# Kernel tuning notes

Measured on AMD Instinct MI355X. Metric: run time of the kernel, lower is better.

## Reference

```python
import jax, jax.numpy as jnp
import numpy as np

N_NODES = 100000
N_EDGES = 1000000
NODE_DIM = 64
EDGE_DIM = 32
N_LAYERS = 4
NUM_GAUSS = EDGE_DIM // 2
HIDDEN = 2 * NODE_DIM
NUM_GRAPHS = 64
VOCAB = 100


def setup_inputs() -> dict:
    key = jax.random.key(0)
    ks = jax.random.split(key, 16)
    atoms = jax.random.randint(ks[0], (N_NODES,), 0, VOCAB, dtype=jnp.int32)
    edge_index = jax.random.randint(ks[1], (2, N_EDGES), 0, N_NODES, dtype=jnp.int32)
    coordinates = jax.random.normal(ks[2], (N_NODES, 3), dtype=jnp.float32) * 2.0
    is_receptor = jax.random.randint(ks[3], (N_NODES,), 0, 2, dtype=jnp.int32)
    batch_ids = jnp.sort(jax.random.randint(ks[4], (N_NODES,), 0, NUM_GRAPHS, dtype=jnp.int32))
    cat_dim = 2 * NODE_DIM + EDGE_DIM  # 160
    node_embed_w = jax.random.normal(ks[5], (VOCAB, NODE_DIM), dtype=jnp.float32) * 0.02
    subunit_embed_w = jax.random.normal(ks[6], (2, EDGE_DIM // 2), dtype=jnp.float32) * 0.02
    W1 = jax.random.normal(ks[7], (N_LAYERS, cat_dim, HIDDEN), dtype=jnp.float32) * (cat_dim ** -0.5)
    b1 = jnp.zeros((N_LAYERS, HIDDEN), dtype=jnp.float32)
    W2 = jax.random.normal(ks[8], (N_LAYERS, HIDDEN, NODE_DIM), dtype=jnp.float32) * (HIDDEN ** -0.5)
    b2 = jnp.zeros((N_LAYERS, NODE_DIM), dtype=jnp.float32)
    fc_w = jax.random.normal(ks[9], (NODE_DIM, 1), dtype=jnp.float32) * (NODE_DIM ** -0.5)
    fc_b = jnp.zeros((1,), dtype=jnp.float32)
    return {"atoms": atoms, "edge_index": edge_index, "coordinates": coordinates,
            "is_receptor": is_receptor, "batch_ids": batch_ids,
            "node_embed_w": node_embed_w, "subunit_embed_w": subunit_embed_w,
            "W1": W1, "b1": b1, "W2": W2, "b2": b2, "fc_w": fc_w, "fc_b": fc_b}


def reference(atoms, edge_index, coordinates, is_receptor, batch_ids,
              node_embed_w, subunit_embed_w, W1, b1, W2, b2, fc_w, fc_b):
    src, dst = edge_index[0], edge_index[1]
    # node embedding
    h = node_embed_w[atoms]  # [N, D]
    # edge attributes: RBF of distance + intermolecular-kind embedding
    offset = jnp.linspace(0.0, 5.0, NUM_GAUSS, dtype=jnp.float32)
    coeff = -0.5 / float(5.0 / (NUM_GAUSS - 1)) ** 2
    dist = jnp.linalg.norm(coordinates[src] - coordinates[dst], axis=1)  # [E]
    rbf = jnp.exp(coeff * (dist[:, None] - offset[None, :]) ** 2)  # [E, G]
    kind = (is_receptor[src] != is_receptor[dst]).astype(jnp.int32)
    edge_attr = jnp.concatenate([rbf, subunit_embed_w[kind]], axis=1)  # [E, EDGE_DIM]
    # message passing layers (PyG source_to_target: h_i = h[dst], h_j = h[src], aggr at dst)
    for l in range(W1.shape[0]):
        m = jnp.concatenate([h[dst], h[src], edge_attr], axis=1)  # [E, 2D+EDGE_DIM]
        m = jax.nn.silu(m @ W1[l] + b1[l]) @ W2[l] + b2[l]  # [E, D]
        agg = jax.ops.segment_sum(m, dst, num_segments=h.shape[0])
        h = jax.nn.relu(h + agg)
    # global mean pool over graphs
    sums = jax.ops.segment_sum(h, batch_ids, num_segments=NUM_GRAPHS)
    counts = jax.ops.segment_sum(jnp.ones((h.shape[0],), h.dtype), batch_ids, num_segments=NUM_GRAPHS)
    pooled = sums / jnp.maximum(counts, 1.0)[:, None]
    out = pooled @ fc_w + fc_b  # [G, 1]
    return out.squeeze(-1)
```

## Files before the change

kernel.cpp:

```cpp
#include <hip/hip_runtime.h>
#include <hip/hip_bf16.h>
#include <math.h>

#define NODE_DIM  64
#define EDGE_DIM  32
#define NUM_GAUSS 16
#define HIDDEN    128
#define CAT_DIM   160
#define TBL_BINS  2048
#define TBL_SCALE 256.0f
#define L1ABSZ    (64 * 256)
#define L2SZ      (HIDDEN * NODE_DIM)
#define TBLSZ     (2 * TBL_BINS * 128)

#define NEG_L2E   (-1.442695040888963f)
#define NEG_LN2   (-0.6931471805599453f)

#define BKT_SH    9
#define BKT_SZ    512
#define NBKT_MAX  1024


typedef __attribute__((ext_vector_type(8))) short short8;
typedef __attribute__((ext_vector_type(4))) short short4v;
typedef __attribute__((ext_vector_type(4))) float float4v;

static __device__ __forceinline__ short f2bf(float x) {
  __hip_bfloat16 h = __float2bfloat16(x);
  return *reinterpret_cast<short*>(&h);
}
static __device__ __forceinline__ float bf2f(short s) {
  return __uint_as_float(((unsigned)(unsigned short)s) << 16);
}
static __device__ __forceinline__ float bflo(unsigned u) { return __uint_as_float(u << 16); }
static __device__ __forceinline__ float bfhi(unsigned u) { return __uint_as_float(u & 0xffff0000u); }

#if defined(__has_builtin) && __has_builtin(__builtin_amdgcn_exp2f)
static __device__ __forceinline__ float hw_exp2(float x) { return __builtin_amdgcn_exp2f(x); }
#else
static __device__ __forceinline__ float hw_exp2(float x) { return exp2f(x); }
#endif

__global__ void k_init(const int* __restrict__ atoms, const float* __restrict__ embed_w,
                       short* __restrict__ hb, int n) {
  int stride = gridDim.x * blockDim.x;
  for (int i = blockIdx.x * blockDim.x + threadIdx.x; i < n; i += stride) {
    int p = i & 63;
    int col = (p & 3) * 16 + (p >> 2);
    hb[i] = f2bf(embed_w[atoms[i >> 6] * NODE_DIM + col]);
  }
}

__global__ void k_zero_f(float* __restrict__ p, int n) {
  int stride = gridDim.x * blockDim.x;
  for (int i = blockIdx.x * blockDim.x + threadIdx.x; i < n; i += stride) p[i] = 0.f;
}
__global__ void k_zero_i(int* __restrict__ p, int n) {
  int i = blockIdx.x * blockDim.x + threadIdx.x;
  if (i < n) p[i] = 0;
}

__global__ __launch_bounds__(256) void k_edge_pre(
    const int* __restrict__ src, const int* __restrict__ dst,
    const float* __restrict__ coords, const int* __restrict__ isr,
    int* __restrict__ rec, int* __restrict__ bkt_total, int E) {
  __shared__ int h[NBKT_MAX];
  for (int i = threadIdx.x; i < NBKT_MAX; i += 256) h[i] = 0;
  __syncthreads();
  int stride = gridDim.x * blockDim.x;
  for (int e = blockIdx.x * blockDim.x + threadIdx.x; e < E; e += stride) {
    int s = src[e], d = dst[e];
    float dx = coords[s*3+0] - coords[d*3+0];
    float dy = coords[s*3+1] - coords[d*3+1];
    float dz = coords[s*3+2] - coords[d*3+2];
    float dist = sqrtf(dx*dx + dy*dy + dz*dz);
    int bin = (int)(dist * TBL_SCALE);
    bin = (bin > TBL_BINS - 1) ? TBL_BINS - 1 : bin;
    int kind = (isr[s] != isr[d]) ? 1 : 0;
    rec[e] = (s << 12) | (kind << 11) | bin;
    atomicAdd(&h[d >> BKT_SH], 1);
  }
  __syncthreads();
  for (int i = threadIdx.x; i < NBKT_MAX; i += 256)
    if (h[i]) atomicAdd(&bkt_total[i], h[i]);
}

__global__ void k_scan_buckets(const int* __restrict__ tot, int* __restrict__ base,
                               int* __restrict__ cur) {
  __shared__ int s[NBKT_MAX];
  int t = threadIdx.x;
  int v = tot[t];
  s[t] = v;
  __syncthreads();
  for (int o = 1; o < NBKT_MAX; o <<= 1) {
    int u = (t >= o) ? s[t - o] : 0;
    __syncthreads();
    s[t] += u;
    __syncthreads();
  }
  int ex = s[t] - v;
  base[t] = ex;
  cur[t]  = ex;
}

__global__ __launch_bounds__(256) void k_passA(
    const int* __restrict__ dst, const int* __restrict__ rec,
    int* __restrict__ bkt_cursor,
    int* __restrict__ tmp_rec, unsigned short* __restrict__ tmp_dl, int E) {
  __shared__ int h[NBKT_MAX];
  __shared__ int c[NBKT_MAX];
  const int tid = threadIdx.x;
  const int chunk = (E + gridDim.x - 1) / gridDim.x;
  const int c0 = blockIdx.x * chunk;
  const int c1 = (c0 + chunk < E) ? c0 + chunk : E;
  for (int i = tid; i < NBKT_MAX; i += 256) h[i] = 0;
  __syncthreads();
  for (int e = c0 + tid; e < c1; e += 256)
    atomicAdd(&h[dst[e] >> BKT_SH], 1);
  __syncthreads();
  for (int i = tid; i < NBKT_MAX; i += 256)
    c[i] = h[i] ? atomicAdd(&bkt_cursor[i], h[i]) : 0;
  __syncthreads();
  for (int e = c0 + tid; e < c1; e += 256) {
    int d = dst[e];
    int p = atomicAdd(&c[d >> BKT_SH], 1);
    tmp_rec[p] = rec[e];
    tmp_dl[p]  = (unsigned short)(d & (BKT_SZ - 1));
  }
}

__global__ __launch_bounds__(256) void k_passB(
    const int* __restrict__ tmp_rec, const unsigned short* __restrict__ tmp_dl,
    const int* __restrict__ bkt_base,
    int* __restrict__ sd_p, int* __restrict__ colptr, int* __restrict__ cnts,
    int N, int E, int nbkt) {
  __shared__ int h[BKT_SZ];
  __shared__ int cur[BKT_SZ];
  __shared__ int ps[256];
  const int tid = threadIdx.x;
  const int b = blockIdx.x;
  const int rb = bkt_base[b];
  const int re = (b == nbkt - 1) ? E : bkt_base[b + 1];

  h[tid] = 0; h[tid + 256] = 0;
  __syncthreads();
  for (int r = rb + tid; r < re; r += 256)
    atomicAdd(&h[tmp_dl[r]], 1);
  __syncthreads();

  int a0 = h[2*tid], a1 = h[2*tid + 1];
  ps[tid] = a0 + a1;
  __syncthreads();
  for (int o = 1; o < 256; o <<= 1) {
    int u = (tid >= o) ? ps[tid - o] : 0;
    __syncthreads();
    ps[tid] += u;
    __syncthreads();
  }
  int e0 = tid ? ps[tid - 1] : 0;
  int g0 = rb + e0;
  int g1 = g0 + a0;
  cur[2*tid]     = g0;
  cur[2*tid + 1] = g1;
  int node0 = b * BKT_SZ + 2*tid;
  if (node0 < N)     { colptr[node0]     = g0; cnts[node0]     = a0; }
  if (node0 + 1 < N) { colptr[node0 + 1] = g1; cnts[node0 + 1] = a1; }
  if (b == 0 && tid == 0) colptr[N] = E;
  __syncthreads();

  for (int r = rb + tid; r < re; r += 256) {
    int dl = tmp_dl[r];
    int p = atomicAdd(&cur[dl], 1);
    sd_p[p] = tmp_rec[r];
  }
}

__global__ void k_tbl(const float* __restrict__ W1, const float* __restrict__ sub_w,
                      short* __restrict__ tbl, int total) {
  int i = blockIdx.x * 256 + threadIdx.x;
  if (i >= total) return;
  int col  = i & 127;
  int idx  = i >> 7;
  int bin  = idx & (TBL_BINS - 1);
  int kind = (idx >> 11) & 1;
  int l    = idx >> 12;
  float dist = ((float)bin + 0.5f) * (1.0f / TBL_SCALE);
  const float* W1c = W1 + (size_t)l * CAT_DIM * HIDDEN + 128 * HIDDEN;
  float acc = 0.f;
  #pragma unroll
  for (int g = 0; g < 16; ++g) {
    float t = dist - (float)g * (1.0f / 3.0f);
    acc += __expf(-4.5f * t * t) * W1c[g * 128 + col];
  }
  #pragma unroll
  for (int g = 0; g < 16; ++g)
    acc += sub_w[kind * 16 + g] * W1c[(16 + g) * 128 + col];
  tbl[(size_t)idx * 128 + (col & 15) * 8 + (col >> 4)] = f2bf(acc * NEG_L2E);
}

__global__ void k_pack_w1ab(const float* __restrict__ W1, short* __restrict__ Wp, int total) {
  int i = blockIdx.x * blockDim.x + threadIdx.x;
  if (i >= total) return;
  int l = i / L1ABSZ, r = i % L1ABSZ;
  int k = r / 256, n = r % 256;
  int kp = (k & 15) * 4 + (k >> 4);
  int kt = kp >> 5, quad = (kp >> 3) & 3, j = kp & 7;
  int srow = (n < 128) ? k : 64 + k;
  int scol = (n < 128) ? n : n - 128;
  Wp[l * L1ABSZ + ((kt*4 + quad) * 256 + n) * 8 + j] =
      f2bf(W1[(size_t)l * CAT_DIM * HIDDEN + srow * HIDDEN + scol] * NEG_L2E);
}
__global__ void k_pack_w2(const float* __restrict__ W, short* __restrict__ Wp, int total) {
  int i = blockIdx.x * blockDim.x + threadIdx.x;
  if (i >= total) return;
  int l = i / L2SZ, r = i % L2SZ;
  int k = r / NODE_DIM, n = r % NODE_DIM;
  int kp = (k & 15) * 8 + (k >> 4);
  int kt = kp >> 5, quad = (kp >> 3) & 3, j = kp & 7;
  Wp[l * L2SZ + ((kt*4 + quad) * NODE_DIM + n) * 8 + j] = f2bf(W[i]);
}

__global__ __launch_bounds__(256, 4) void k_node(
    short* __restrict__ hb,
    const short* __restrict__ Sb, const int* __restrict__ cnts,
    const short* __restrict__ W2p, const float* __restrict__ b2,
    const short* __restrict__ W1abp, const float* __restrict__ b1,
    short* __restrict__ pa, short* __restrict__ pb, int N)
{
  __shared__ short ht[64 * 72];

  const int tid  = threadIdx.x;
  const int lane = tid & 63;
  const int w    = tid >> 6;
  const int quad = lane >> 4;
  const int l16  = lane & 15;
  const int base = blockIdx.x * 64 + w * 16;

  if (W2p) {
    float4v acc[4];
    #pragma unroll
    for (int nt = 0; nt < 4; ++nt) acc[nt] = (float4v)0.f;
    const int arow = base + l16;
    const bool av = arow < N;
    #pragma unroll
    for (int kt = 0; kt < 4; ++kt) {
      short8 a = av ? *(const short8*)&Sb[(size_t)arow * 128 + kt*32 + quad*8]
                    : (short8)0;
      #pragma unroll
      for (int nt = 0; nt < 4; ++nt) {
        short8 b = *(const short8*)&W2p[((kt*4 + quad) * NODE_DIM + nt*16 + l16) * 8];
        acc[nt] = __builtin_amdgcn_mfma_f32_16x16x32_bf16(a, b, acc[nt], 0, 0, 0);
      }
    }
    float bb[4];
    #pragma unroll
    for (int nt = 0; nt < 4; ++nt) bb[nt] = b2[nt*16 + l16];
    #pragma unroll
    for (int r = 0; r < 4; ++r) {
      int row  = base + quad*4 + r;
      int lrow = w*16 + quad*4 + r;
      if (row < N) {
        float cf = (float)cnts[row];
        short4v hv = *(const short4v*)&hb[(size_t)row * 64 + l16*4];
        float v0 = fmaxf(bf2f(hv[0]) + acc[0][r] + cf * bb[0], 0.f);
        float v1 = fmaxf(bf2f(hv[1]) + acc[1][r] + cf * bb[1], 0.f);
        float v2 = fmaxf(bf2f(hv[2]) + acc[2][r] + cf * bb[2], 0.f);
        float v3 = fmaxf(bf2f(hv[3]) + acc[3][r] + cf * bb[3], 0.f);
        short4v hs = {f2bf(v0), f2bf(v1), f2bf(v2), f2bf(v3)};
        *(short4v*)&hb[(size_t)row * 64 + l16*4] = hs;
        *(short4v*)&ht[lrow * 72 + l16*4] = hs;
      } else {
        *(short4v*)&ht[lrow * 72 + l16*4] = (short4v)0;
      }
    }
  } else {
    int row = base + l16;
    #pragma unroll
    for (int c = 0; c < 2; ++c) {
      int colc = quad*16 + c*8;
      short8 v = (row < N) ? *(const short8*)&hb[(size_t)row * 64 + colc] : (short8)0;
      *(short8*)&ht[(w*16 + l16) * 72 + colc] = v;
    }
  }

  if (W1abp) {
    float4v acc[16];
    #pragma unroll
    for (int nt = 0; nt < 16; ++nt) acc[nt] = (float4v)0.f;
    #pragma unroll
    for (int kt = 0; kt < 2; ++kt) {
      short8 a = *(const short8*)&ht[(w*16 + l16) * 72 + kt*32 + quad*8];
      #pragma unroll
      for (int nt = 0; nt < 16; ++nt) {
        short8 b = *(const short8*)&W1abp[((kt*4 + quad) * 256 + nt*16 + l16) * 8];
        acc[nt] = __builtin_amdgcn_mfma_f32_16x16x32_bf16(a, b, acc[nt], 0, 0, 0);
      }
    }
    float b1a[8];
    #pragma unroll
    for (int nt = 0; nt < 8; ++nt) b1a[nt] = b1[nt*16 + l16] * NEG_L2E;
    #pragma unroll
    for (int r = 0; r < 4; ++r) {
      int row = base + quad*4 + r;
      if (row < N) {
        short8 va, vb;
        #pragma unroll
        for (int nt = 0; nt < 8; ++nt) va[nt] = f2bf(acc[nt][r] + b1a[nt]);
        #pragma unroll
        for (int nt = 0; nt < 8; ++nt) vb[nt] = f2bf(acc[nt + 8][r]);
        *(short8*)&pa[(size_t)row * 128 + l16*8] = va;
        *(short8*)&pb[(size_t)row * 128 + l16*8] = vb;
      }
    }
  }
}

__global__ __launch_bounds__(256, 8) void k_gather(
    const short* __restrict__ pa, const short* __restrict__ pb,
    const short* __restrict__ tblL,
    const int* __restrict__ sd_p, const int* __restrict__ colptr,
    short* __restrict__ Sb, int N)
{
  const int W   = gridDim.x * 4;
  const int wid = blockIdx.x * 4 + (threadIdx.x >> 6);
  const int lane = threadIdx.x & 63;
  const int d2 = lane * 2;
  const int d4 = lane * 4;

  const char* pbB = (const char*)pb;
  const char* tbB = (const char*)tblL;

  for (int n = wid; n < N; n += W) {
    const int s = __builtin_amdgcn_readfirstlane(colptr[n]);
    const int e = __builtin_amdgcn_readfirstlane(colptr[n + 1]);

    unsigned up = *(const unsigned*)&pa[(size_t)n * 128 + d2];
    const float p0 = bflo(up), p1 = bfhi(up);
    float s0 = 0.f, s1 = 0.f;

    if (e > s) {
      unsigned ub0[4], ue0[4], ub1[4], ue1[4];

      auto load4 = [&](unsigned (&ub)[4], unsigned (&ue)[4], int j) {
        #pragma unroll
        for (int t = 0; t < 4; ++t) {
          int jj = (j + t < e) ? j + t : s;
          int rc = __builtin_amdgcn_readfirstlane(sd_p[jj]);
          const char* pr = pbB + ((size_t)((unsigned)rc >> 12) << 8);
          const char* tr = tbB + ((size_t)(rc & 0xfff) << 8);
          ub[t] = *(const unsigned*)(pr + d4);
          ue[t] = *(const unsigned*)(tr + d4);
        }
      };
      auto consume4 = [&](unsigned (&ub)[4], unsigned (&ue)[4], int j) {
        #pragma unroll
        for (int t = 0; t < 4; ++t) {
          if (j + t < e) {
            float y0 = p0 + bflo(ub[t]) + bflo(ue[t]);
            float y1 = p1 + bfhi(ub[t]) + bfhi(ue[t]);
            s0 += y0 * __builtin_amdgcn_rcpf(1.f + hw_exp2(y0));
            s1 += y1 * __builtin_amdgcn_rcpf(1.f + hw_exp2(y1));
          }
        }
      };

      load4(ub0, ue0, s);
      int j = s;
      for (; j + 4 < e; j += 8) {
        load4(ub1, ue1, j + 4);
        consume4(ub0, ue0, j);
        if (j + 8 < e) load4(ub0, ue0, j + 8);
        consume4(ub1, ue1, j + 4);
      }
      if (j < e) consume4(ub0, ue0, j);
    }

    s0 *= NEG_LN2;
    s1 *= NEG_LN2;
    unsigned pk = ((unsigned)(unsigned short)f2bf(s1) << 16) | (unsigned short)f2bf(s0);
    *(unsigned*)&Sb[(size_t)n * 128 + d2] = pk;
  }
}

__global__ void k_pool(const short* __restrict__ hb, const int* __restrict__ batch_ids,
                       float* __restrict__ pooled, float* __restrict__ counts, int N) {
  int lane = threadIdx.x & 63;
  int base = blockIdx.x * 64;
  float acc = 0.f;
  int   cnt = 0;
  int  gcur = -1;
  for (int n = 0; n < 64; ++n) {
    int node = base + n;
    if (node >= N) break;
    int g = batch_ids[node];
    if (g != gcur) {
      if (gcur >= 0) {
        atomicAdd(&pooled[gcur * NODE_DIM + lane], acc);
        if (lane == 0) atomicAdd(&counts[gcur], (float)cnt);
      }
      gcur = g; acc = 0.f; cnt = 0;
    }
    acc += bf2f(hb[(size_t)node * NODE_DIM + lane]);
    cnt++;
  }
  if (gcur >= 0) {
    atomicAdd(&pooled[gcur * NODE_DIM + lane], acc);
    if (lane == 0) atomicAdd(&counts[gcur], (float)cnt);
  }
}

__global__ void k_final(const float* __restrict__ pooled, const float* __restrict__ counts,
                        const float* __restrict__ fc_w, const float* __restrict__ fc_b,
                        float* __restrict__ out, int G) {
  int g = blockIdx.x * blockDim.x + threadIdx.x;
  if (g < G) {
    float acc = 0.f;
    for (int d = 0; d < NODE_DIM; ++d) {
      int col = (d & 3) * 16 + (d >> 2);
      acc += pooled[g * NODE_DIM + d] * fc_w[col];
    }
    float c = counts[g];
    if (c < 1.f) c = 1.f;
    out[g] = acc / c + fc_b[0];
  }
}

extern "C" void kernel_launch(void* const* d_in, const int* in_sizes, int n_in,
                              void* d_out, int out_size, void* d_ws, size_t ws_size,
                              hipStream_t stream) {
  const int*   atoms   = (const int*)  d_in[0];
  const int*   eidx    = (const int*)  d_in[1];
  const float* coords  = (const float*)d_in[2];
  const int*   isr     = (const int*)  d_in[3];
  const int*   batch   = (const int*)  d_in[4];
  const float* embed_w = (const float*)d_in[5];
  const float* sub_w   = (const float*)d_in[6];
  const float* W1      = (const float*)d_in[7];
  const float* b1      = (const float*)d_in[8];
  const float* W2      = (const float*)d_in[9];
  const float* b2      = (const float*)d_in[10];
  const float* fc_w    = (const float*)d_in[11];
  const float* fc_b    = (const float*)d_in[12];
  float* out = (float*)d_out;

  const int N = in_sizes[0];
  const int E = in_sizes[1] / 2;
  const int L = in_sizes[8] / HIDDEN;
  const int G = out_size;

  const int* srcv = eidx;
  const int* dstv = eidx + E;

  size_t off = 0;
  auto carve = [&](size_t bytes) -> char* {
    char* p = (char*)d_ws + off;
    off += (bytes + 255) & ~(size_t)255;
    return p;
  };
  short* hb       = (short*)carve((size_t)N * NODE_DIM * 2);
  short* Sb       = (short*)carve((size_t)N * HIDDEN * 2);
  short* pa       = (short*)carve((size_t)N * HIDDEN * 2);
  short* pb       = (short*)carve((size_t)N * HIDDEN * 2);
  int*   rec      = (int*)  carve((size_t)E * 4);
  int*   sd_p     = (int*)  carve((size_t)E * 4);
  int*   tmp_rec  = (int*)  carve((size_t)E * 4);
  unsigned short* tmp_dl = (unsigned short*)carve((size_t)E * 2);
  int*   cnts     = (int*)  carve((size_t)N * 4);
  int*   colptr   = (int*)  carve(((size_t)N + 2) * 4);
  int*   bkt_total  = (int*)carve((size_t)NBKT_MAX * 4);
  int*   bkt_base   = (int*)carve((size_t)(NBKT_MAX + 1) * 4);
  int*   bkt_cursor = (int*)carve((size_t)NBKT_MAX * 4);
  short* W1abp    = (short*)carve((size_t)L * L1ABSZ * 2);
  short* W2p      = (short*)carve((size_t)L * L2SZ * 2);
  short* tbl      = (short*)carve((size_t)L * TBLSZ * 2);
  float* pooled   = (float*)carve((size_t)G * NODE_DIM * 4);
  float* cntg     = (float*)carve((size_t)G * 4);

  const int nbkt = (N + BKT_SZ - 1) / BKT_SZ;

  k_zero_i<<<(NBKT_MAX + 255) / 256, 256, 0, stream>>>(bkt_total, NBKT_MAX);
  k_init<<<1024, 256, 0, stream>>>(atoms, embed_w, hb, N * NODE_DIM);
  k_edge_pre<<<512, 256, 0, stream>>>(srcv, dstv, coords, isr, rec, bkt_total, E);
  k_zero_f<<<(G * NODE_DIM + G + 255) / 256, 256, 0, stream>>>(pooled, G * NODE_DIM + G);
  k_scan_buckets<<<1, NBKT_MAX, 0, stream>>>(bkt_total, bkt_base, bkt_cursor);
  k_passA<<<256, 256, 0, stream>>>(dstv, rec, bkt_cursor, tmp_rec, tmp_dl, E);
  k_passB<<<nbkt, 256, 0, stream>>>(tmp_rec, tmp_dl, bkt_base, sd_p, colptr, cnts, N, E, nbkt);
  k_pack_w1ab<<<(L * L1ABSZ + 255) / 256, 256, 0, stream>>>(W1, W1abp, L * L1ABSZ);
  k_pack_w2<<<(L * L2SZ + 255) / 256, 256, 0, stream>>>(W2, W2p, L * L2SZ);
  k_tbl<<<(L * 2 * TBL_BINS * 128 + 255) / 256, 256, 0, stream>>>(W1, sub_w, tbl,
                                                                  L * 2 * TBL_BINS * 128);

  const int nblk_n = (N + 63) / 64;
  const int nblk_g = 2048;
  for (int l = 0; l < L; ++l) {
    k_node<<<nblk_n, 256, 0, stream>>>(
        hb, Sb, cnts,
        (l > 0) ? W2p + (size_t)(l - 1) * L2SZ : (const short*)nullptr,
        (l > 0) ? b2 + (size_t)(l - 1) * NODE_DIM : (const float*)nullptr,
        W1abp + (size_t)l * L1ABSZ, b1 + (size_t)l * HIDDEN,
        pa, pb, N);
    k_gather<<<nblk_g, 256, 0, stream>>>(pa, pb, tbl + (size_t)l * TBLSZ,
                                         sd_p, colptr, Sb, N);
  }
  k_node<<<nblk_n, 256, 0, stream>>>(
      hb, Sb, cnts,
      W2p + (size_t)(L - 1) * L2SZ, b2 + (size_t)(L - 1) * NODE_DIM,
      (const short*)nullptr, (const float*)nullptr, pa, pb, N);

  k_pool<<<(N + 63) / 64, 64, 0, stream>>>(hb, batch, pooled, cntg, N);
  k_final<<<1, 64, 0, stream>>>(pooled, cntg, fc_w, fc_b, out, G);
}
```

Before: 543.6 us.

## Fuse edge gather with node update and next-layer projection

```diff
diff --git a/kernel.cpp b/kernel.cpp
--- a/kernel.cpp
+++ b/kernel.cpp
@@ -236,44 +236,7 @@
   const int l16  = lane & 15;
   const int base = blockIdx.x * 64 + w * 16;
 
-  if (W2p) {
-    float4v acc[4];
-    #pragma unroll
-    for (int nt = 0; nt < 4; ++nt) acc[nt] = (float4v)0.f;
-    const int arow = base + l16;
-    const bool av = arow < N;
-    #pragma unroll
-    for (int kt = 0; kt < 4; ++kt) {
-      short8 a = av ? *(const short8*)&Sb[(size_t)arow * 128 + kt*32 + quad*8]
-                    : (short8)0;
-      #pragma unroll
-      for (int nt = 0; nt < 4; ++nt) {
-        short8 b = *(const short8*)&W2p[((kt*4 + quad) * NODE_DIM + nt*16 + l16) * 8];
-        acc[nt] = __builtin_amdgcn_mfma_f32_16x16x32_bf16(a, b, acc[nt], 0, 0, 0);
-      }
-    }
-    float bb[4];
-    #pragma unroll
-    for (int nt = 0; nt < 4; ++nt) bb[nt] = b2[nt*16 + l16];
-    #pragma unroll
-    for (int r = 0; r < 4; ++r) {
-      int row  = base + quad*4 + r;
-      int lrow = w*16 + quad*4 + r;
-      if (row < N) {
-        float cf = (float)cnts[row];
-        short4v hv = *(const short4v*)&hb[(size_t)row * 64 + l16*4];
-        float v0 = fmaxf(bf2f(hv[0]) + acc[0][r] + cf * bb[0], 0.f);
-        float v1 = fmaxf(bf2f(hv[1]) + acc[1][r] + cf * bb[1], 0.f);
-        float v2 = fmaxf(bf2f(hv[2]) + acc[2][r] + cf * bb[2], 0.f);
-        float v3 = fmaxf(bf2f(hv[3]) + acc[3][r] + cf * bb[3], 0.f);
-        short4v hs = {f2bf(v0), f2bf(v1), f2bf(v2), f2bf(v3)};
-        *(short4v*)&hb[(size_t)row * 64 + l16*4] = hs;
-        *(short4v*)&ht[lrow * 72 + l16*4] = hs;
-      } else {
-        *(short4v*)&ht[lrow * 72 + l16*4] = (short4v)0;
-      }
-    }
-  } else {
+  {
     int row = base + l16;
     #pragma unroll
     for (int c = 0; c < 2; ++c) {
@@ -315,22 +278,35 @@
   }
 }
 
-__global__ __launch_bounds__(256, 8) void k_gather(
-    const short* __restrict__ pa, const short* __restrict__ pb,
+__global__ __launch_bounds__(256, 4) void k_fused(
+    short* __restrict__ hb, const int* __restrict__ cnts,
+    const short* __restrict__ pa, const short* __restrict__ pbin,
     const short* __restrict__ tblL,
     const int* __restrict__ sd_p, const int* __restrict__ colptr,
-    short* __restrict__ Sb, int N)
+    const short* __restrict__ W2p, const float* __restrict__ b2,
+    const short* __restrict__ W1abp, const float* __restrict__ b1,
+    short* __restrict__ pa_out, short* __restrict__ pb_out, int N)
 {
-  const int W   = gridDim.x * 4;
-  const int wid = blockIdx.x * 4 + (threadIdx.x >> 6);
-  const int lane = threadIdx.x & 63;
-  const int d2 = lane * 2;
-  const int d4 = lane * 4;
-
-  const char* pbB = (const char*)pb;
+  __shared__ short sbt[64 * 136];
+  __shared__ short ht[64 * 72];
+
+  const int tid  = threadIdx.x;
+  const int lane = tid & 63;
+  const int w    = tid >> 6;
+  const int quad = lane >> 4;
+  const int l16  = lane & 15;
+  const int base = blockIdx.x * 64 + w * 16;
+  const int d2   = lane * 2;
+  const int d4   = lane * 4;
+
+  const char* pbB = (const char*)pbin;
   const char* tbB = (const char*)tblL;
 
-  for (int n = wid; n < N; n += W) {
+  for (int i = 0; i < 16; ++i) {
+    const int n = base + i;
+    unsigned* ldst = (unsigned*)&sbt[(w*16 + i) * 136 + d2];
+    if (n >= N) { *ldst = 0u; continue; }
+
     const int s = __builtin_amdgcn_readfirstlane(colptr[n]);
     const int e = __builtin_amdgcn_readfirstlane(colptr[n + 1]);
 
@@ -377,8 +353,74 @@
 
     s0 *= NEG_LN2;
     s1 *= NEG_LN2;
-    unsigned pk = ((unsigned)(unsigned short)f2bf(s1) << 16) | (unsigned short)f2bf(s0);
-    *(unsigned*)&Sb[(size_t)n * 128 + d2] = pk;
+    *ldst = ((unsigned)(unsigned short)f2bf(s1) << 16) | (unsigned short)f2bf(s0);
+  }
+
+  {
+    float4v acc[4];
+    #pragma unroll
+    for (int nt = 0; nt < 4; ++nt) acc[nt] = (float4v)0.f;
+    #pragma unroll
+    for (int kt = 0; kt < 4; ++kt) {
+      short8 a = *(const short8*)&sbt[(w*16 + l16) * 136 + kt*32 + quad*8];
+      #pragma unroll
+      for (int nt = 0; nt < 4; ++nt) {
+        short8 b = *(const short8*)&W2p[((kt*4 + quad) * NODE_DIM + nt*16 + l16) * 8];
+        acc[nt] = __builtin_amdgcn_mfma_f32_16x16x32_bf16(a, b, acc[nt], 0, 0, 0);
+      }
+    }
+    float bb[4];
+    #pragma unroll
+    for (int nt = 0; nt < 4; ++nt) bb[nt] = b2[nt*16 + l16];
+    #pragma unroll
+    for (int r = 0; r < 4; ++r) {
+      int row  = base + quad*4 + r;
+      int lrow = w*16 + quad*4 + r;
+      if (row < N) {
+        float cf = (float)cnts[row];
+        short4v hv = *(const short4v*)&hb[(size_t)row * 64 + l16*4];
+        float v0 = fmaxf(bf2f(hv[0]) + acc[0][r] + cf * bb[0], 0.f);
+        float v1 = fmaxf(bf2f(hv[1]) + acc[1][r] + cf * bb[1], 0.f);
+        float v2 = fmaxf(bf2f(hv[2]) + acc[2][r] + cf * bb[2], 0.f);
+        float v3 = fmaxf(bf2f(hv[3]) + acc[3][r] + cf * bb[3], 0.f);
+        short4v hs = {f2bf(v0), f2bf(v1), f2bf(v2), f2bf(v3)};
+        *(short4v*)&hb[(size_t)row * 64 + l16*4] = hs;
+        *(short4v*)&ht[lrow * 72 + l16*4] = hs;
+      } else {
+        *(short4v*)&ht[lrow * 72 + l16*4] = (short4v)0;
+      }
+    }
+  }
+
+  if (W1abp) {
+    float4v acc[16];
+    #pragma unroll
+    for (int nt = 0; nt < 16; ++nt) acc[nt] = (float4v)0.f;
+    #pragma unroll
+    for (int kt = 0; kt < 2; ++kt) {
+      short8 a = *(const short8*)&ht[(w*16 + l16) * 72 + kt*32 + quad*8];
+      #pragma unroll
+      for (int nt = 0; nt < 16; ++nt) {
+        short8 b = *(const short8*)&W1abp[((kt*4 + quad) * 256 + nt*16 + l16) * 8];
+        acc[nt] = __builtin_amdgcn_mfma_f32_16x16x32_bf16(a, b, acc[nt], 0, 0, 0);
+      }
+    }
+    float b1a[8];
+    #pragma unroll
+    for (int nt = 0; nt < 8; ++nt) b1a[nt] = b1[nt*16 + l16] * NEG_L2E;
+    #pragma unroll
+    for (int r = 0; r < 4; ++r) {
+      int row = base + quad*4 + r;
+      if (row < N) {
+        short8 va, vb;
+        #pragma unroll
+        for (int nt = 0; nt < 8; ++nt) va[nt] = f2bf(acc[nt][r] + b1a[nt]);
+        #pragma unroll
+        for (int nt = 0; nt < 8; ++nt) vb[nt] = f2bf(acc[nt + 8][r]);
+        *(short8*)&pa_out[(size_t)row * 128 + l16*8] = va;
+        *(short8*)&pb_out[(size_t)row * 128 + l16*8] = vb;
+      }
+    }
   }
 }
 
@@ -458,9 +500,9 @@
     return p;
   };
   short* hb       = (short*)carve((size_t)N * NODE_DIM * 2);
-  short* Sb       = (short*)carve((size_t)N * HIDDEN * 2);
   short* pa       = (short*)carve((size_t)N * HIDDEN * 2);
-  short* pb       = (short*)carve((size_t)N * HIDDEN * 2);
+  short* pb0      = (short*)carve((size_t)N * HIDDEN * 2);
+  short* pb1      = (short*)carve((size_t)N * HIDDEN * 2);
   int*   rec      = (int*)  carve((size_t)E * 4);
   int*   sd_p     = (int*)  carve((size_t)E * 4);
   int*   tmp_rec  = (int*)  carve((size_t)E * 4);
@@ -491,21 +533,24 @@
                                                                   L * 2 * TBL_BINS * 128);
 
   const int nblk_n = (N + 63) / 64;
-  const int nblk_g = 2048;
+
+  k_node<<<nblk_n, 256, 0, stream>>>(
+      hb, (const short*)nullptr, (const int*)nullptr,
+      (const short*)nullptr, (const float*)nullptr,
+      W1abp, b1, pa, pb0, N);
+
   for (int l = 0; l < L; ++l) {
-    k_node<<<nblk_n, 256, 0, stream>>>(
-        hb, Sb, cnts,
-        (l > 0) ? W2p + (size_t)(l - 1) * L2SZ : (const short*)nullptr,
-        (l > 0) ? b2 + (size_t)(l - 1) * NODE_DIM : (const float*)nullptr,
-        W1abp + (size_t)l * L1ABSZ, b1 + (size_t)l * HIDDEN,
-        pa, pb, N);
-    k_gather<<<nblk_g, 256, 0, stream>>>(pa, pb, tbl + (size_t)l * TBLSZ,
-                                         sd_p, colptr, Sb, N);
-  }
-  k_node<<<nblk_n, 256, 0, stream>>>(
-      hb, Sb, cnts,
-      W2p + (size_t)(L - 1) * L2SZ, b2 + (size_t)(L - 1) * NODE_DIM,
-      (const short*)nullptr, (const float*)nullptr, pa, pb, N);
+    short* pbin  = (l & 1) ? pb1 : pb0;
+    short* pbout = (l & 1) ? pb0 : pb1;
+    const bool last = (l == L - 1);
+    k_fused<<<nblk_n, 256, 0, stream>>>(
+        hb, cnts, pa, pbin,
+        tbl + (size_t)l * TBLSZ, sd_p, colptr,
+        W2p + (size_t)l * L2SZ, b2 + (size_t)l * NODE_DIM,
+        last ? (const short*)nullptr : W1abp + (size_t)(l + 1) * L1ABSZ,
+        last ? (const float*)nullptr : b1 + (size_t)(l + 1) * HIDDEN,
+        pa, pbout, N);
+  }
 
   k_pool<<<(N + 63) / 64, 64, 0, stream>>>(hb, batch, pooled, cntg, N);
   k_final<<<1, 64, 0, stream>>>(pooled, cntg, fc_w, fc_b, out, G);
```

After: 594.7 us. 9.4% more time.
